# Kernel optimization log

Hardware: AMD Instinct MI355X
Metric: run time of the kernel (lower is better)

Reference implementation:

```python
import jax, jax.numpy as jnp
import numpy as np

N_AQI, N_MEO = 35, 18
F_OUT = 16
ALPHA = 0.2


def _xavier(k, shape, gain=1.414):
    fan_in, fan_out = shape
    limit = gain * (6.0 / (fan_in + fan_out)) ** 0.5
    return jax.random.uniform(k, shape, jnp.float32, -limit, limit)


def setup_inputs() -> dict:
    key = jax.random.key(0)
    ks = jax.random.split(key, 16)
    B, T = 32, 32
    N = N_AQI + N_MEO
    out_aqi = jax.random.normal(ks[0], (B, T, N_AQI, 1), jnp.float32)
    out_meo = jax.random.normal(ks[1], (B, T, N_MEO, 3), jnp.float32)
    # sparse-ish adjacency with self loops; adj_norm is a (masked) float weight
    adj = (jax.random.uniform(ks[2], (N, N)) < 0.3).astype(jnp.float32)
    adj = adj.at[jnp.arange(N), jnp.arange(N)].set(1.0)
    adj_norm = adj * jax.random.uniform(ks[3], (N, N), jnp.float32)
    inp = {
        "out_aqi": out_aqi,
        "out_meo": out_meo,
        "adj": adj,
        "adj_norm": adj_norm,
        "W_trans": _xavier(ks[4], (1, 6), gain=1.0),
        "b_trans": jnp.zeros((6,), jnp.float32),
        "W_xa": _xavier(ks[5], (6, F_OUT)),
        "W_xm": _xavier(ks[6], (3, F_OUT)),
        "W_ua": _xavier(ks[7], (6, F_OUT)),
        "W_um": _xavier(ks[8], (3, F_OUT)),
        "a_aa": _xavier(ks[9], (2 * F_OUT + 1, 1)),
        "a_am": _xavier(ks[10], (2 * F_OUT + 1, 1)),
        "a_ma": _xavier(ks[11], (2 * F_OUT + 1, 1)),
        "a_mm": _xavier(ks[12], (2 * F_OUT + 1, 1)),
        "W_out": _xavier(ks[13], (32, 1), gain=1.0),
        "b_out": jnp.zeros((1,), jnp.float32),
    }
    return inp


def _lrelu(x):
    return jnp.where(x > 0, x, ALPHA * x)


def _edge_block(h_src, h_dst, anorm_blk, a):
    # Equivalent to matmul(cat[h_i, h_j, adj_norm_ij], a) without materializing
    # the dense (BT, Ni, Nj, 2F+1) tensor: split a into src/dst/adj parts.
    s = h_src @ a[:F_OUT, 0]                 # (BT, Ni)
    d = h_dst @ a[F_OUT:2 * F_OUT, 0]        # (BT, Nj)
    return _lrelu(s[:, :, None] + d[:, None, :] + anorm_blk[None, :, :] * a[2 * F_OUT, 0])


def reference(out_aqi, out_meo, adj, adj_norm, W_trans, b_trans, W_xa, W_xm,
              W_ua, W_um, a_aa, a_am, a_ma, a_mm, W_out, b_out):
    B, T = out_aqi.shape[:2]
    BT = B * T
    aqi = out_aqi.reshape(BT, N_AQI, 1) @ W_trans + b_trans    # (BT, 35, 6)
    meo = out_meo.reshape(BT, N_MEO, 3)                         # (BT, 18, 3)

    heter_attri = jnp.concatenate([aqi @ W_xa, meo @ W_xm], axis=1)  # (BT, 53, 16)
    h_aqi = aqi @ W_ua                                          # (BT, 35, 16)
    h_meo = meo @ W_um                                          # (BT, 18, 16)

    an = adj_norm
    e_aa = _edge_block(h_aqi, h_aqi, an[:N_AQI, :N_AQI], a_aa)
    e_am = _edge_block(h_aqi, h_meo, an[:N_AQI, N_AQI:], a_am)
    e_ma = _edge_block(h_meo, h_aqi, an[N_AQI:, :N_AQI], a_ma)
    e_mm = _edge_block(h_meo, h_meo, an[N_AQI:, N_AQI:], a_mm)
    e = jnp.concatenate([
        jnp.concatenate([e_aa, e_am], axis=2),
        jnp.concatenate([e_ma, e_mm], axis=2),
    ], axis=1)                                                  # (BT, 53, 53)

    att = jnp.where(adj[None, :, :] > 0, e, -1e12)
    att = jax.nn.softmax(att, axis=2)
    heter_out = att @ heter_attri                               # (BT, 53, 16)

    m_aqi = jnp.mean(heter_out[:, :N_AQI, :], axis=1)
    m_meo = jnp.mean(heter_out[:, N_AQI:, :], axis=1)
    out_smetric = jax.nn.sigmoid(jnp.concatenate([m_aqi, m_meo], axis=1))  # (BT, 32)
    out_sscore = jax.nn.sigmoid(out_smetric @ W_out + b_out)               # (BT, 1)
    return out_sscore, out_smetric
```

## Files before the change

### kernel.cpp

```cpp
#include <hip/hip_runtime.h>

#define N_AQI 35
#define N_MEO 18
#define NN    53
#define F     16

__global__ __launch_bounds__(64)
void spat_disc_kernel(
    const float* __restrict__ out_aqi,
    const float* __restrict__ out_meo,
    const float* __restrict__ adj,
    const float* __restrict__ adj_norm,
    const float* __restrict__ W_trans,
    const float* __restrict__ b_trans,
    const float* __restrict__ W_xa,
    const float* __restrict__ W_xm,
    const float* __restrict__ W_ua,
    const float* __restrict__ W_um,
    const float* __restrict__ a_aa,
    const float* __restrict__ a_am,
    const float* __restrict__ a_ma,
    const float* __restrict__ a_mm,
    const float* __restrict__ W_out,
    const float* __restrict__ b_out,
    float* __restrict__ out, int BT)
{
  const int bt  = blockIdx.x;
  const int tid = threadIdx.x;

  __shared__ float sh_wxa[F], sh_bxa[F], sh_wua[F], sh_bua[F];
  __shared__ float sh_c[8];
  __shared__ float sh_v[12];
  __shared__ float sh_l[4];
  __shared__ float sh_attri[NN * 17];
  __shared__ float sh_d[2 * N_AQI + 2 * N_MEO];
  __shared__ float sh_e[NN * NN];
  __shared__ float sh_ho[NN * 17];
  __shared__ float sh_sm[32];

  if (tid < F) {
    float wxa = 0.f, bxa = 0.f, wua = 0.f, bua = 0.f;
    for (int k = 0; k < 6; ++k) {
      float wt = W_trans[k], btr = b_trans[k];
      wxa += wt  * W_xa[k * F + tid];
      bxa += btr * W_xa[k * F + tid];
      wua += wt  * W_ua[k * F + tid];
      bua += btr * W_ua[k * F + tid];
    }
    sh_wxa[tid] = wxa; sh_bxa[tid] = bxa;
    sh_wua[tid] = wua; sh_bua[tid] = bua;
  }
  __syncthreads();

  if (tid < 8) {
    const float* avec = (tid == 0 || tid == 1 || tid == 4 || tid == 5) ? a_aa
                       : (tid < 4 ? a_am : a_ma);
    int off = (tid < 4) ? 0 : F;
    const float* wv = (tid & 1) ? sh_bua : sh_wua;
    float acc = 0.f;
    for (int f = 0; f < F; ++f) acc += wv[f] * avec[off + f];
    sh_c[tid] = acc;
  } else if (tid < 20) {
    int t = tid - 8;
    int k = t % 3;
    int grp = t / 3;
    const float* avec = (grp == 0) ? a_ma : (grp == 1) ? a_mm
                       : (grp == 2) ? a_am : a_mm;
    int off = (grp < 2) ? 0 : F;
    float acc = 0.f;
    for (int f = 0; f < F; ++f) acc += W_um[k * F + f] * avec[off + f];
    sh_v[t] = acc;
  } else if (tid < 24) {
    const float* avec = (tid == 20) ? a_aa : (tid == 21) ? a_am
                       : (tid == 22) ? a_ma : a_mm;
    sh_l[tid - 20] = avec[2 * F];
  }
  __syncthreads();

  float s_a = 0.f, s_m = 0.f, l_a = 0.f, l_m = 0.f;
  if (tid < N_AQI) {
    float x = out_aqi[bt * N_AQI + tid];
    s_a = sh_c[0] * x + sh_c[1];
    s_m = sh_c[2] * x + sh_c[3];
    sh_d[tid]         = sh_c[4] * x + sh_c[5];
    sh_d[N_AQI + tid] = sh_c[6] * x + sh_c[7];
    for (int f = 0; f < F; ++f)
      sh_attri[tid * 17 + f] = sh_wxa[f] * x + sh_bxa[f];
    l_a = sh_l[0]; l_m = sh_l[1];
  } else if (tid < NN) {
    int m = tid - N_AQI;
    float m0 = out_meo[(bt * N_MEO + m) * 3 + 0];
    float m1 = out_meo[(bt * N_MEO + m) * 3 + 1];
    float m2 = out_meo[(bt * N_MEO + m) * 3 + 2];
    s_a = m0 * sh_v[0] + m1 * sh_v[1]  + m2 * sh_v[2];
    s_m = m0 * sh_v[3] + m1 * sh_v[4]  + m2 * sh_v[5];
    sh_d[2 * N_AQI + m]         = m0 * sh_v[6] + m1 * sh_v[7]  + m2 * sh_v[8];
    sh_d[2 * N_AQI + N_MEO + m] = m0 * sh_v[9] + m1 * sh_v[10] + m2 * sh_v[11];
    for (int f = 0; f < F; ++f)
      sh_attri[tid * 17 + f] = m0 * W_xm[0 * F + f] + m1 * W_xm[1 * F + f] + m2 * W_xm[2 * F + f];
    l_a = sh_l[2]; l_m = sh_l[3];
  }
  __syncthreads();

  if (tid < NN) {
    const int i = tid;
    const float* adj_row = adj + i * NN;
    const float* an_row  = adj_norm + i * NN;
    float mx = -1e30f;
    for (int j = 0; j < NN; ++j) {
      float e;
      if (adj_row[j] > 0.0f) {
        float dv = (j < N_AQI)
                     ? ((i < N_AQI) ? sh_d[j] : sh_d[N_AQI + j])
                     : ((i < N_AQI) ? sh_d[2 * N_AQI + (j - N_AQI)]
                                    : sh_d[2 * N_AQI + N_MEO + (j - N_AQI)]);
        float sv = (j < N_AQI) ? s_a : s_m;
        float lv = (j < N_AQI) ? l_a : l_m;
        float z = sv + dv + an_row[j] * lv;
        e = (z > 0.0f) ? z : 0.2f * z;
        if (e > mx) mx = e;
      } else {
        e = -INFINITY;
      }
      sh_e[i * NN + j] = e;
    }
    float acc[F];
#pragma unroll
    for (int f = 0; f < F; ++f) acc[f] = 0.f;
    float lsum = 0.f;
    for (int j = 0; j < NN; ++j) {
      float w = __expf(sh_e[i * NN + j] - mx);
      lsum += w;
#pragma unroll
      for (int f = 0; f < F; ++f) acc[f] += w * sh_attri[j * 17 + f];
    }
    float inv = 1.0f / lsum;
#pragma unroll
    for (int f = 0; f < F; ++f) sh_ho[i * 17 + f] = acc[f] * inv;
  }
  __syncthreads();

  if (tid < 32) {
    float s = 0.f;
    if (tid < F) {
      for (int i = 0; i < N_AQI; ++i) s += sh_ho[i * 17 + tid];
      s *= (1.0f / N_AQI);
    } else {
      int f = tid - F;
      for (int i = N_AQI; i < NN; ++i) s += sh_ho[i * 17 + f];
      s *= (1.0f / N_MEO);
    }
    float sm = 1.0f / (1.0f + __expf(-s));
    sh_sm[tid] = sm;
    out[BT + bt * 32 + tid] = sm;
  }
  __syncthreads();

  if (tid == 0) {
    float z = b_out[0];
    for (int k = 0; k < 32; ++k) z += sh_sm[k] * W_out[k];
    out[bt] = 1.0f / (1.0f + __expf(-z));
  }
}

extern "C" void kernel_launch(void* const* d_in, const int* in_sizes, int n_in,
                              void* d_out, int out_size, void* d_ws, size_t ws_size,
                              hipStream_t stream) {
  const float* out_aqi  = (const float*)d_in[0];
  const float* out_meo  = (const float*)d_in[1];
  const float* adj      = (const float*)d_in[2];
  const float* adj_norm = (const float*)d_in[3];
  const float* W_trans  = (const float*)d_in[4];
  const float* b_trans  = (const float*)d_in[5];
  const float* W_xa     = (const float*)d_in[6];
  const float* W_xm     = (const float*)d_in[7];
  const float* W_ua     = (const float*)d_in[8];
  const float* W_um     = (const float*)d_in[9];
  const float* a_aa     = (const float*)d_in[10];
  const float* a_am     = (const float*)d_in[11];
  const float* a_ma     = (const float*)d_in[12];
  const float* a_mm     = (const float*)d_in[13];
  const float* W_out    = (const float*)d_in[14];
  const float* b_out    = (const float*)d_in[15];
  float* out = (float*)d_out;

  const int BT = in_sizes[0] / N_AQI;

  spat_disc_kernel<<<BT, 64, 0, stream>>>(
      out_aqi, out_meo, adj, adj_norm, W_trans, b_trans,
      W_xa, W_xm, W_ua, W_um, a_aa, a_am, a_ma, a_mm, W_out, b_out,
      out, BT);
}
```

Measured before the change: 110.3 us.

## Split attention rows across four threads and drop max-subtraction in softmax

Raises the block from 64 to 256 threads so each attention row is handled by four threads, each accumulating four of the sixteen output features through float4 shared-memory loads. The masked adjacency times the per-block attention scalar is precomputed cooperatively into shared memory. The separate max pass and the stored edge matrix are removed, so exponentials are taken directly without max-subtraction. This cuts the serial per-thread loop work, at the risk of overflow in the exponent if edge logits are large.

```diff
diff --git a/kernel.cpp b/kernel.cpp
--- a/kernel.cpp
+++ b/kernel.cpp
@@ -4,8 +4,9 @@
 #define N_MEO 18
 #define NN    53
 #define F     16
+#define AP    20
 
-__global__ __launch_bounds__(64)
+__global__ __launch_bounds__(256)
 void spat_disc_kernel(
     const float* __restrict__ out_aqi,
     const float* __restrict__ out_meo,
@@ -27,15 +28,18 @@
 {
   const int bt  = blockIdx.x;
   const int tid = threadIdx.x;
+  const int i   = tid >> 2;
+  const int fq  = tid & 3;
 
   __shared__ float sh_wxa[F], sh_bxa[F], sh_wua[F], sh_bua[F];
   __shared__ float sh_c[8];
   __shared__ float sh_v[12];
   __shared__ float sh_l[4];
-  __shared__ float sh_attri[NN * 17];
-  __shared__ float sh_d[2 * N_AQI + 2 * N_MEO];
-  __shared__ float sh_e[NN * NN];
-  __shared__ float sh_ho[NN * 17];
+  __shared__ float sh_dA[NN];
+  __shared__ float sh_dM[NN];
+  __shared__ float sh_attri[NN * AP];
+  __shared__ float sh_P[NN * NN];
+  __shared__ float sh_ho[NN * AP];
   __shared__ float sh_sm[32];
 
   if (tid < F) {
@@ -77,77 +81,77 @@
   }
   __syncthreads();
 
-  float s_a = 0.f, s_m = 0.f, l_a = 0.f, l_m = 0.f;
-  if (tid < N_AQI) {
-    float x = out_aqi[bt * N_AQI + tid];
-    s_a = sh_c[0] * x + sh_c[1];
-    s_m = sh_c[2] * x + sh_c[3];
-    sh_d[tid]         = sh_c[4] * x + sh_c[5];
-    sh_d[N_AQI + tid] = sh_c[6] * x + sh_c[7];
-    for (int f = 0; f < F; ++f)
-      sh_attri[tid * 17 + f] = sh_wxa[f] * x + sh_bxa[f];
-    l_a = sh_l[0]; l_m = sh_l[1];
-  } else if (tid < NN) {
-    int m = tid - N_AQI;
-    float m0 = out_meo[(bt * N_MEO + m) * 3 + 0];
-    float m1 = out_meo[(bt * N_MEO + m) * 3 + 1];
-    float m2 = out_meo[(bt * N_MEO + m) * 3 + 2];
-    s_a = m0 * sh_v[0] + m1 * sh_v[1]  + m2 * sh_v[2];
-    s_m = m0 * sh_v[3] + m1 * sh_v[4]  + m2 * sh_v[5];
-    sh_d[2 * N_AQI + m]         = m0 * sh_v[6] + m1 * sh_v[7]  + m2 * sh_v[8];
-    sh_d[2 * N_AQI + N_MEO + m] = m0 * sh_v[9] + m1 * sh_v[10] + m2 * sh_v[11];
-    for (int f = 0; f < F; ++f)
-      sh_attri[tid * 17 + f] = m0 * W_xm[0 * F + f] + m1 * W_xm[1 * F + f] + m2 * W_xm[2 * F + f];
-    l_a = sh_l[2]; l_m = sh_l[3];
+  if (tid < NN) {
+    if (tid < N_AQI) {
+      float x = out_aqi[bt * N_AQI + tid];
+      sh_dA[tid] = sh_c[4] * x + sh_c[5];
+      sh_dM[tid] = sh_c[6] * x + sh_c[7];
+      for (int f = 0; f < F; ++f)
+        sh_attri[tid * AP + f] = sh_wxa[f] * x + sh_bxa[f];
+    } else {
+      int m = tid - N_AQI;
+      float m0 = out_meo[(bt * N_MEO + m) * 3 + 0];
+      float m1 = out_meo[(bt * N_MEO + m) * 3 + 1];
+      float m2 = out_meo[(bt * N_MEO + m) * 3 + 2];
+      sh_dA[tid] = m0 * sh_v[6] + m1 * sh_v[7]  + m2 * sh_v[8];
+      sh_dM[tid] = m0 * sh_v[9] + m1 * sh_v[10] + m2 * sh_v[11];
+      for (int f = 0; f < F; ++f)
+        sh_attri[tid * AP + f] = m0 * W_xm[0 * F + f] + m1 * W_xm[1 * F + f] + m2 * W_xm[2 * F + f];
+    }
+  }
+  for (int t = tid; t < NN * NN; t += 256) {
+    int ii = t / NN;
+    int jj = t - ii * NN;
+    float a  = adj[t];
+    float an = adj_norm[t];
+    float l  = (ii < N_AQI) ? ((jj < N_AQI) ? sh_l[0] : sh_l[1])
+                            : ((jj < N_AQI) ? sh_l[2] : sh_l[3]);
+    sh_P[t] = (a > 0.f) ? an * l : -INFINITY;
+  }
+  float s0 = 0.f, s1 = 0.f;
+  if (i < NN) {
+    if (i < N_AQI) {
+      float x = out_aqi[bt * N_AQI + i];
+      s0 = sh_c[0] * x + sh_c[1];
+      s1 = sh_c[2] * x + sh_c[3];
+    } else {
+      int m = i - N_AQI;
+      float m0 = out_meo[(bt * N_MEO + m) * 3 + 0];
+      float m1 = out_meo[(bt * N_MEO + m) * 3 + 1];
+      float m2 = out_meo[(bt * N_MEO + m) * 3 + 2];
+      s0 = m0 * sh_v[0] + m1 * sh_v[1] + m2 * sh_v[2];
+      s1 = m0 * sh_v[3] + m1 * sh_v[4] + m2 * sh_v[5];
+    }
   }
   __syncthreads();
 
-  if (tid < NN) {
-    const int i = tid;
-    const float* adj_row = adj + i * NN;
-    const float* an_row  = adj_norm + i * NN;
-    float mx = -1e30f;
+  if (i < NN) {
+    const float* dbase = (i < N_AQI) ? sh_dA : sh_dM;
+    const float* Prow  = sh_P + i * NN;
+    float a0 = 0.f, a1 = 0.f, a2 = 0.f, a3 = 0.f, lsum = 0.f;
+#pragma unroll 1
     for (int j = 0; j < NN; ++j) {
-      float e;
-      if (adj_row[j] > 0.0f) {
-        float dv = (j < N_AQI)
-                     ? ((i < N_AQI) ? sh_d[j] : sh_d[N_AQI + j])
-                     : ((i < N_AQI) ? sh_d[2 * N_AQI + (j - N_AQI)]
-                                    : sh_d[2 * N_AQI + N_MEO + (j - N_AQI)]);
-        float sv = (j < N_AQI) ? s_a : s_m;
-        float lv = (j < N_AQI) ? l_a : l_m;
-        float z = sv + dv + an_row[j] * lv;
-        e = (z > 0.0f) ? z : 0.2f * z;
-        if (e > mx) mx = e;
-      } else {
-        e = -INFINITY;
-      }
-      sh_e[i * NN + j] = e;
-    }
-    float acc[F];
-#pragma unroll
-    for (int f = 0; f < F; ++f) acc[f] = 0.f;
-    float lsum = 0.f;
-    for (int j = 0; j < NN; ++j) {
-      float w = __expf(sh_e[i * NN + j] - mx);
+      float z = ((j < N_AQI) ? s0 : s1) + dbase[j] + Prow[j];
+      float e = (z > 0.0f) ? z : 0.2f * z;
+      float w = __expf(e);
       lsum += w;
-#pragma unroll
-      for (int f = 0; f < F; ++f) acc[f] += w * sh_attri[j * 17 + f];
+      const float4 av = *(const float4*)(sh_attri + j * AP + fq * 4);
+      a0 += w * av.x; a1 += w * av.y; a2 += w * av.z; a3 += w * av.w;
     }
     float inv = 1.0f / lsum;
-#pragma unroll
-    for (int f = 0; f < F; ++f) sh_ho[i * 17 + f] = acc[f] * inv;
+    float4* hrow = (float4*)(sh_ho + i * AP + fq * 4);
+    *hrow = make_float4(a0 * inv, a1 * inv, a2 * inv, a3 * inv);
   }
   __syncthreads();
 
   if (tid < 32) {
     float s = 0.f;
     if (tid < F) {
-      for (int i = 0; i < N_AQI; ++i) s += sh_ho[i * 17 + tid];
+      for (int r = 0; r < N_AQI; ++r) s += sh_ho[r * AP + tid];
       s *= (1.0f / N_AQI);
     } else {
       int f = tid - F;
-      for (int i = N_AQI; i < NN; ++i) s += sh_ho[i * 17 + f];
+      for (int r = N_AQI; r < NN; ++r) s += sh_ho[r * AP + f];
       s *= (1.0f / N_MEO);
     }
     float sm = 1.0f / (1.0f + __expf(-s));
@@ -186,7 +190,7 @@
 
   const int BT = in_sizes[0] / N_AQI;
 
-  spat_disc_kernel<<<BT, 64, 0, stream>>>(
+  spat_disc_kernel<<<BT, 256, 0, stream>>>(
       out_aqi, out_meo, adj, adj_norm, W_trans, b_trans,
       W_xa, W_xm, W_ua, W_um, a_aa, a_am, a_ma, a_mm, W_out, b_out,
       out, BT);
```

Result: faster. 99.18 us (-10.1%).
